# Kernel optimization log

Hardware: AMD Instinct MI355X
Metric: run time of the kernel (lower is better)

Reference implementation:

```python
import jax, jax.numpy as jnp
import numpy as np

B, L, V, E, H, K, T = 256, 49, 10000, 512, 512, 512, 15


def setup_inputs() -> dict:
    key = jax.random.key(0)
    ks = jax.random.split(key, 16)
    s = 0.02
    return {
        "features": jax.random.normal(ks[0], (B, L, K), dtype=jnp.float32),
        "captions": jax.random.randint(ks[1], (B, T), 0, V),
        "emb": jax.random.normal(ks[2], (V, E), dtype=jnp.float32) * s,
        "Wq": jax.random.normal(ks[3], (H, H), dtype=jnp.float32) * s,
        "bq": jnp.zeros((H,), jnp.float32),
        "Uk": jax.random.normal(ks[4], (H, K), dtype=jnp.float32) * s,
        "bk": jnp.zeros((H,), jnp.float32),
        "Va": jax.random.normal(ks[5], (1, H), dtype=jnp.float32) * s,
        "bva": jnp.zeros((1,), jnp.float32),
        "W0": jax.random.normal(ks[6], (H, K), dtype=jnp.float32) * s,
        "b0": jnp.zeros((H,), jnp.float32),
        "Wih": jax.random.normal(ks[7], (3 * H, E + H), dtype=jnp.float32) * s,
        "bih": jnp.zeros((3 * H,), jnp.float32),
        "Whh": jax.random.normal(ks[8], (3 * H, H), dtype=jnp.float32) * s,
        "bhh": jnp.zeros((3 * H,), jnp.float32),
        "W1": jax.random.normal(ks[9], (V, H), dtype=jnp.float32) * s,
        "b1": jnp.zeros((V,), jnp.float32),
    }


def reference(features, captions, emb, Wq, bq, Uk, bk, Va, bva, W0, b0, Wih, bih, Whh, bhh, W1, b1):
    # embeddings: [B, T, E]
    embeddings = emb[captions]
    # precompute key projection for additive attention: [B, L, H]
    keys_proj = jnp.einsum("blk,hk->blh", features, Uk) + bk

    def step(h, emb_t):  # h: [B,H], emb_t: [B,E]
        q = h @ Wq.T + bq                                  # [B, H]
        scores = jnp.tanh(q[:, None, :] + keys_proj) @ Va.T + bva  # [B, L, 1]
        w = jax.nn.softmax(scores, axis=1)                 # [B, L, 1]
        ctx = jnp.sum(w * features, axis=1)                # [B, K]
        ctx = ctx @ W0.T + b0                              # [B, H]
        x = jnp.concatenate([emb_t, ctx], axis=-1)         # [B, E+H]
        gi = x @ Wih.T + bih                               # [B, 3H]
        gh = h @ Whh.T + bhh                               # [B, 3H]
        i_r, i_z, i_n = jnp.split(gi, 3, axis=-1)
        h_r, h_z, h_n = jnp.split(gh, 3, axis=-1)
        r = jax.nn.sigmoid(i_r + h_r)
        z = jax.nn.sigmoid(i_z + h_z)
        n = jnp.tanh(i_n + r * h_n)
        h_new = (1.0 - z) * n + z * h
        out = h_new @ W1.T + b1                            # [B, V]
        return h_new, out

    h0 = jnp.zeros((features.shape[0], H), features.dtype)
    _, outs = jax.lax.scan(step, h0, jnp.swapaxes(embeddings, 0, 1))  # [T, B, V]
    return jnp.swapaxes(outs, 0, 1)  # [B, T, V]
```

## Files before the change

kernel.cpp:

```cpp
#include <hip/hip_runtime.h>
#include <hip/hip_bf16.h>
#include <math.h>

#define B_ 256
#define L_ 49
#define V_ 10000
#define E_ 512
#define H_ 512
#define K_ 512
#define T_ 15

typedef __bf16 bf16x8 __attribute__((ext_vector_type(8)));
typedef float f32x4 __attribute__((ext_vector_type(4)));

#define AS1 __attribute__((address_space(1)))
#define AS3 __attribute__((address_space(3)))

__device__ __forceinline__ float tanh_fast(float x)
{
    const float ax = fabsf(x);
    const float e = __expf(2.f * ax);
    const float t = 1.f - 2.f / (e + 1.f);
    return copysignf(t, x);
}

struct CvtSegs {
    const float* src[6];
    __hip_bfloat16* dst[6];
    int blk_end[6];
};

__global__ __launch_bounds__(256) void cvt_multi_kernel(CvtSegs s)
{
    const int blk = blockIdx.x;
    int seg = 0;
    while (blk >= s.blk_end[seg]) ++seg;
    const int base = seg ? s.blk_end[seg - 1] : 0;
    const int i = (blk - base) * 256 + threadIdx.x;
    const float4 v = ((const float4*)s.src[seg])[i];
    __hip_bfloat16 o[4];
    o[0] = (__hip_bfloat16)v.x; o[1] = (__hip_bfloat16)v.y;
    o[2] = (__hip_bfloat16)v.z; o[3] = (__hip_bfloat16)v.w;
    *(ushort4*)(s.dst[seg] + (size_t)i * 4) = *(ushort4*)o;
}

__global__ __launch_bounds__(256) void transpose_cast_kernel(
    const float* __restrict__ in, __hip_bfloat16* __restrict__ out, int R, int Cc)
{
    __shared__ float tile[32][33];
    const int tr0 = blockIdx.y * 32, tc0 = blockIdx.x * 32;
    const int tx = threadIdx.x & 31, ty = threadIdx.x >> 5;
#pragma unroll
    for (int i = 0; i < 32; i += 8)
        tile[ty + i][tx] = in[(size_t)(tr0 + ty + i) * Cc + tc0 + tx];
    __syncthreads();
#pragma unroll
    for (int i = 0; i < 32; i += 8)
        out[(size_t)(tc0 + ty + i) * R + tr0 + tx] = (__hip_bfloat16)tile[tx][ty + i];
}

__global__ __launch_bounds__(256) void bfull_kernel(
    const float* __restrict__ Wih, const float* __restrict__ b0,
    const float* __restrict__ bih, float* __restrict__ bfull)
{
    const int i = blockIdx.x * 256 + threadIdx.x;
    if (i >= 3 * H_) return;
    const float* wrow = Wih + (size_t)i * (E_ + H_) + E_;
    float acc = bih[i];
    for (int j = 0; j < H_; ++j) acc += wrow[j] * b0[j];
    bfull[i] = acc;
}

__global__ __launch_bounds__(128) void emb_gather_kernel(
    const int* __restrict__ caps, const float* __restrict__ emb,
    __hip_bfloat16* __restrict__ out)
{
    const int r = blockIdx.x;
    const int t = r >> 8;
    const int b = r & 255;
    const int cap = caps[(size_t)b * T_ + t];
    const int e = threadIdx.x * 4;
    const float4 v = *(const float4*)(emb + (size_t)cap * E_ + e);
    __hip_bfloat16 o[4];
    o[0] = (__hip_bfloat16)v.x; o[1] = (__hip_bfloat16)v.y;
    o[2] = (__hip_bfloat16)v.z; o[3] = (__hip_bfloat16)v.w;
    *(ushort4*)(out + (size_t)r * E_ + e) = *(ushort4*)o;
}

template <typename OutT>
__global__ __launch_bounds__(256) void gemm_bf16_nt128_kernel(
    const __hip_bfloat16* __restrict__ A, const __hip_bfloat16* __restrict__ Bw,
    const float* __restrict__ bias, OutT* __restrict__ C,
    int N, int Kd, int lda, int ldb, int ldc, int nby)
{
    int wg = blockIdx.x;
    {
        const int nwg = gridDim.x;
        const int q = nwg >> 3, r = nwg & 7;
        const int xcd = wg & 7, idx = wg >> 3;
        wg = (xcd < r ? xcd * (q + 1) : r * (q + 1) + (xcd - r) * q) + idx;
    }
    const int by = wg % nby;
    const int bx = wg / nby;
    const int row0 = by * 128;
    const int col0 = bx * 128;

    __shared__ __hip_bfloat16 Asl[128 * 64];
    __shared__ __hip_bfloat16 Bsl[128 * 64];
    const int tid  = threadIdx.x;
    const int lane = tid & 63;
    const int w    = tid >> 6;
    const int wm   = w >> 1, wn = w & 1;

    const int srow = tid >> 3;
    const int scol = (tid & 7) << 3;

    const int lr = lane & 15;
    const int lk = (lane >> 4) << 3;

    f32x4 acc[4][4] = {};

    const __hip_bfloat16* gA = A + (size_t)(row0 + srow) * lda + scol;
    bool bv[4];
    const __hip_bfloat16* gB[4];
#pragma unroll
    for (int i = 0; i < 4; ++i) {
        const int br = col0 + i * 32 + srow;
        bv[i] = br < N;
        gB[i] = Bw + (size_t)br * ldb + scol;
    }

    for (int k0 = 0; k0 < Kd; k0 += 64) {
        __syncthreads();
#pragma unroll
        for (int i = 0; i < 4; ++i)
            __builtin_amdgcn_global_load_lds((const AS1 void*)(gA + (size_t)i * 32 * lda + k0),
                (AS3 void*)(Asl + i * 2048 + tid * 8), 16, 0, 0);
#pragma unroll
        for (int i = 0; i < 4; ++i)
            if (bv[i]) __builtin_amdgcn_global_load_lds((const AS1 void*)(gB[i] + k0),
                (AS3 void*)(Bsl + i * 2048 + tid * 8), 16, 0, 0);
        __syncthreads();

#pragma unroll
        for (int ks = 0; ks < 2; ++ks) {
            bf16x8 af[4], bfr[4];
#pragma unroll
            for (int i = 0; i < 4; ++i)
                af[i] = *(const bf16x8*)(Asl + (wm * 64 + i * 16 + lr) * 64 + ks * 32 + lk);
#pragma unroll
            for (int j = 0; j < 4; ++j)
                bfr[j] = *(const bf16x8*)(Bsl + (wn * 64 + j * 16 + lr) * 64 + ks * 32 + lk);
#pragma unroll
            for (int i = 0; i < 4; ++i)
#pragma unroll
                for (int j = 0; j < 4; ++j)
                    acc[i][j] = __builtin_amdgcn_mfma_f32_16x16x32_bf16(
                        af[i], bfr[j], acc[i][j], 0, 0, 0);
        }
    }

    const int orow = (lane >> 4) << 2;
#pragma unroll
    for (int i = 0; i < 4; ++i) {
#pragma unroll
        for (int j = 0; j < 4; ++j) {
            const int col = col0 + wn * 64 + j * 16 + lr;
            if (col >= N) continue;
            const float bvv = bias ? bias[col] : 0.f;
            const int rowb = row0 + wm * 64 + i * 16 + orow;
#pragma unroll
            for (int r = 0; r < 4; ++r)
                C[(size_t)(rowb + r) * ldc + col] = (OutT)(acc[i][j][r] + bvv);
        }
    }
}

template <typename OutT, typename CinT>
__device__ __forceinline__ void gemm_nt_body(
    const __hip_bfloat16* __restrict__ A, const __hip_bfloat16* __restrict__ Bw,
    const float* __restrict__ bias, const CinT* __restrict__ Cin, int ldcin,
    OutT* __restrict__ C, int M, int N, int Kd, int lda, int ldb, int ldc,
    int bx, int by)
{
    __shared__ __hip_bfloat16 Asl[2][64 * 64];
    __shared__ __hip_bfloat16 Bsl[2][64 * 64];
    const int tid  = threadIdx.x;
    const int lane = tid & 63;
    const int w    = tid >> 6;
    const int wm   = w >> 1, wn = w & 1;
    const int row0 = by * 64;
    const int col0 = bx * 64;

    const int srow = tid >> 3;
    const int scol = (tid & 7) << 3;

    const int lr = lane & 15;
    const int lk = (lane >> 4) << 3;

    f32x4 acc[2][2] = {};

    const __hip_bfloat16* gA0 = A + (size_t)(row0 + srow) * lda + scol;
    const __hip_bfloat16* gA1 = gA0 + (size_t)32 * lda;
    const int br0 = col0 + srow, br1 = br0 + 32;
    const __hip_bfloat16* gB0 = Bw + (size_t)br0 * ldb + scol;
    const __hip_bfloat16* gB1 = gB0 + (size_t)32 * ldb;
    const bool v0 = br0 < N, v1 = br1 < N;

    auto stage = [&](int buf, int k0) {
        __builtin_amdgcn_global_load_lds((const AS1 void*)(gA0 + k0),
            (AS3 void*)(&Asl[buf][tid * 8]), 16, 0, 0);
        __builtin_amdgcn_global_load_lds((const AS1 void*)(gA1 + k0),
            (AS3 void*)(&Asl[buf][2048 + tid * 8]), 16, 0, 0);
        if (v0) __builtin_amdgcn_global_load_lds((const AS1 void*)(gB0 + k0),
            (AS3 void*)(&Bsl[buf][tid * 8]), 16, 0, 0);
        if (v1) __builtin_amdgcn_global_load_lds((const AS1 void*)(gB1 + k0),
            (AS3 void*)(&Bsl[buf][2048 + tid * 8]), 16, 0, 0);
    };

    stage(0, 0);
    __syncthreads();
    int cur = 0;
    for (int k0 = 0; k0 < Kd; k0 += 64) {
        if (k0 + 64 < Kd) stage(cur ^ 1, k0 + 64);

#pragma unroll
        for (int ks = 0; ks < 2; ++ks) {
            bf16x8 af[2], bfr[2];
#pragma unroll
            for (int i = 0; i < 2; ++i)
                af[i] = *(const bf16x8*)(&Asl[cur][(wm * 32 + i * 16 + lr) * 64 + ks * 32 + lk]);
#pragma unroll
            for (int j = 0; j < 2; ++j)
                bfr[j] = *(const bf16x8*)(&Bsl[cur][(wn * 32 + j * 16 + lr) * 64 + ks * 32 + lk]);
#pragma unroll
            for (int i = 0; i < 2; ++i)
#pragma unroll
                for (int j = 0; j < 2; ++j)
                    acc[i][j] = __builtin_amdgcn_mfma_f32_16x16x32_bf16(
                        af[i], bfr[j], acc[i][j], 0, 0, 0);
        }
        __syncthreads();
        cur ^= 1;
    }

    const int orow = (lane >> 4) << 2;
#pragma unroll
    for (int i = 0; i < 2; ++i) {
#pragma unroll
        for (int j = 0; j < 2; ++j) {
            const int col = col0 + wn * 32 + j * 16 + lr;
            if (col >= N) continue;
            const float bvv = bias ? bias[col] : 0.f;
            const int rowb = row0 + wm * 32 + i * 16 + orow;
#pragma unroll
            for (int r = 0; r < 4; ++r) {
                float v = acc[i][j][r] + bvv;
                if (Cin) v += (float)Cin[(size_t)(rowb + r) * ldcin + col];
                C[(size_t)(rowb + r) * ldc + col] = (OutT)v;
            }
        }
    }
}

__global__ __launch_bounds__(256) void gemm_gigh_kernel(
    const __hip_bfloat16* __restrict__ ctx, const __hip_bfloat16* __restrict__ Wf,
    const __hip_bfloat16* __restrict__ gi_emb_t,
    const __hip_bfloat16* __restrict__ hb, const __hip_bfloat16* __restrict__ Whh,
    const float* __restrict__ bhh,
    __hip_bfloat16* __restrict__ gi, __hip_bfloat16* __restrict__ gh)
{
    if (blockIdx.z == 0)
        gemm_nt_body<__hip_bfloat16, __hip_bfloat16>(
            ctx, Wf, nullptr, gi_emb_t, 3 * H_, gi,
            B_, 3 * H_, K_, K_, K_, 3 * H_, blockIdx.x, blockIdx.y);
    else
        gemm_nt_body<__hip_bfloat16, float>(
            hb, Whh, bhh, (const float*)nullptr, 0, gh,
            B_, 3 * H_, H_, H_, H_, 3 * H_, blockIdx.x, blockIdx.y);
}

__global__ __launch_bounds__(512) void attn_gru_kernel(
    const __hip_bfloat16* __restrict__ gi, const __hip_bfloat16* __restrict__ gh,
    float* __restrict__ h, __hip_bfloat16* __restrict__ hb,
    __hip_bfloat16* __restrict__ h_all, int tprev,
    const __hip_bfloat16* __restrict__ WqT, const float* __restrict__ bq,
    const __hip_bfloat16* __restrict__ kp, const __hip_bfloat16* __restrict__ feat,
    const float* __restrict__ Va, const float* __restrict__ bva,
    __hip_bfloat16* __restrict__ ctx)
{
    const int b = blockIdx.x;
    const int tid = threadIdx.x;
    const int lane = tid & 63;
    const int wave = tid >> 6;
    __shared__ float hb_s[H_];
    __shared__ float q_part[8][H_];
    __shared__ float q_s[H_];
    __shared__ float s_sc[64];
    __shared__ float s_w[64];

    if (tprev >= 0) {
        const int j = tid;
        const size_t o = (size_t)b * (3 * H_) + j;
        const float ir = (float)gi[o],           hr = (float)gh[o];
        const float iz = (float)gi[o + H_],      hz = (float)gh[o + H_];
        const float in_ = (float)gi[o + 2 * H_], hn = (float)gh[o + 2 * H_];
        const float rr = 1.f / (1.f + expf(-(ir + hr)));
        const float zz = 1.f / (1.f + expf(-(iz + hz)));
        const float nn = tanhf(in_ + rr * hn);
        const size_t hi = (size_t)b * H_ + j;
        const float hnew = (1.f - zz) * nn + zz * h[hi];
        h[hi] = hnew;
        hb_s[j] = hnew;
        const __hip_bfloat16 hv = (__hip_bfloat16)hnew;
        hb[hi] = hv;
        h_all[((size_t)b * T_ + tprev) * H_ + j] = hv;
    } else {
        hb_s[tid] = 0.f;
    }
    __syncthreads();

    {
        const int j0 = lane * 8;
        float accq[8] = {};
        const __hip_bfloat16* wbase = WqT + (size_t)(wave * 64) * H_ + j0;
#pragma unroll 16
        for (int k = 0; k < 64; ++k) {
            const float hv = hb_s[wave * 64 + k];
            const bf16x8 wv = *(const bf16x8*)(wbase + (size_t)k * H_);
#pragma unroll
            for (int i = 0; i < 8; ++i) accq[i] = fmaf(hv, (float)wv[i], accq[i]);
        }
#pragma unroll
        for (int i = 0; i < 8; ++i) q_part[wave][j0 + i] = accq[i];
    }
    __syncthreads();
    {
        const int j = tid;
        float s = bq[j];
#pragma unroll
        for (int w2 = 0; w2 < 8; ++w2) s += q_part[w2][j];
        q_s[j] = s;
    }
    __syncthreads();

    float qr[8], va[8];
#pragma unroll
    for (int i = 0; i < 8; ++i) {
        qr[i] = q_s[lane * 8 + i];
        va[i] = Va[lane * 8 + i];
    }

    for (int l = wave; l < L_; l += 8) {
        const bf16x8 kv = *(const bf16x8*)(kp + ((size_t)b * L_ + l) * H_ + lane * 8);
        float s = 0.f;
#pragma unroll
        for (int i = 0; i < 8; ++i) s += tanh_fast(qr[i] + (float)kv[i]) * va[i];
#pragma unroll
        for (int off = 32; off > 0; off >>= 1) s += __shfl_xor(s, off, 64);
        if (lane == 0) s_sc[l] = s + bva[0];
    }
    __syncthreads();

    if (wave == 0) {
        const float v = (lane < L_) ? s_sc[lane] : -1e30f;
        float m = v;
#pragma unroll
        for (int off = 32; off > 0; off >>= 1) m = fmaxf(m, __shfl_xor(m, off, 64));
        const float e = (lane < L_) ? expf(v - m) : 0.f;
        float ssum = e;
#pragma unroll
        for (int off = 32; off > 0; off >>= 1) ssum += __shfl_xor(ssum, off, 64);
        if (lane < L_) s_w[lane] = e / ssum;
    }
    __syncthreads();

    {
        float acc0 = 0.f;
        const __hip_bfloat16* fb = feat + (size_t)b * L_ * K_ + tid;
#pragma unroll 7
        for (int l = 0; l < L_; ++l)
            acc0 = fmaf(s_w[l], (float)fb[(size_t)l * K_], acc0);
        ctx[(size_t)b * K_ + tid] = (__hip_bfloat16)acc0;
    }
}

__global__ __launch_bounds__(256) void gru_kernel(
    const __hip_bfloat16* __restrict__ gi, const __hip_bfloat16* __restrict__ gh,
    float* __restrict__ h, __hip_bfloat16* __restrict__ hb,
    __hip_bfloat16* __restrict__ h_all, int t)
{
    const int idx = blockIdx.x * 256 + threadIdx.x;
    const int b = idx >> 9;
    const int j = idx & (H_ - 1);
    const size_t o = (size_t)b * 3 * H_ + j;
    const float ir = (float)gi[o],           hr = (float)gh[o];
    const float iz = (float)gi[o + H_],      hz = (float)gh[o + H_];
    const float in_ = (float)gi[o + 2 * H_], hn = (float)gh[o + 2 * H_];
    const float r = 1.f / (1.f + expf(-(ir + hr)));
    const float z = 1.f / (1.f + expf(-(iz + hz)));
    const float n = tanhf(in_ + r * hn);
    const float hnew = (1.f - z) * n + z * h[idx];
    h[idx] = hnew;
    const __hip_bfloat16 hv = (__hip_bfloat16)hnew;
    hb[idx] = hv;
    h_all[((size_t)b * T_ + t) * H_ + j] = hv;
}

extern "C" void kernel_launch(void* const* d_in, const int* in_sizes, int n_in,
                              void* d_out, int out_size, void* d_ws, size_t ws_size,
                              hipStream_t stream)
{
    const float* features = (const float*)d_in[0];
    const int*   captions = (const int*)d_in[1];
    const float* emb  = (const float*)d_in[2];
    const float* Wq   = (const float*)d_in[3];
    const float* bq   = (const float*)d_in[4];
    const float* Uk   = (const float*)d_in[5];
    const float* bk   = (const float*)d_in[6];
    const float* Va   = (const float*)d_in[7];
    const float* bva  = (const float*)d_in[8];
    const float* W0   = (const float*)d_in[9];
    const float* b0   = (const float*)d_in[10];
    const float* Wih  = (const float*)d_in[11];
    const float* bih  = (const float*)d_in[12];
    const float* Whh  = (const float*)d_in[13];
    const float* bhh  = (const float*)d_in[14];
    const float* W1   = (const float*)d_in[15];
    const float* b1   = (const float*)d_in[16];
    float* out = (float*)d_out;

    float* ws = (float*)d_ws;
    float* h      = ws; ws += B_ * H_;
    float* bfull  = ws; ws += 3 * H_;
    __hip_bfloat16* bws = (__hip_bfloat16*)ws;
    __hip_bfloat16* gi      = bws; bws += (size_t)B_ * 3 * H_;
    __hip_bfloat16* gh      = bws; bws += (size_t)B_ * 3 * H_;
    __hip_bfloat16* gi_emb  = bws; bws += (size_t)T_ * B_ * 3 * H_;
    __hip_bfloat16* feat_bf = bws; bws += (size_t)B_ * L_ * K_;
    __hip_bfloat16* kp_bf   = bws; bws += (size_t)B_ * L_ * H_;
    __hip_bfloat16* W1_bf   = bws; bws += (size_t)V_ * H_;
    __hip_bfloat16* Uk_bf   = bws; bws += (size_t)H_ * K_;
    __hip_bfloat16* WqT_bf  = bws; bws += (size_t)H_ * H_;
    __hip_bfloat16* W0T_bf  = bws; bws += (size_t)K_ * H_;
    __hip_bfloat16* Wih_bf  = bws; bws += (size_t)3 * H_ * (E_ + H_);
    __hip_bfloat16* Whh_bf  = bws; bws += (size_t)3 * H_ * H_;
    __hip_bfloat16* Wfused  = bws; bws += (size_t)3 * H_ * K_;
    __hip_bfloat16* emb_all = bws; bws += (size_t)T_ * B_ * E_;
    __hip_bfloat16* hb      = bws; bws += (size_t)B_ * H_;
    __hip_bfloat16* ctx_bf  = bws; bws += (size_t)B_ * K_;
    __hip_bfloat16* h_all   = bws; bws += (size_t)B_ * T_ * H_;

    hipMemsetAsync(h, 0, (size_t)B_ * H_ * sizeof(float), stream);
    hipMemsetAsync(hb, 0, (size_t)B_ * H_ * sizeof(__hip_bfloat16), stream);

    const dim3 blk(256);

    {
        CvtSegs s;
        s.src[0] = features; s.dst[0] = feat_bf;
        s.src[1] = W1;       s.dst[1] = W1_bf;
        s.src[2] = Uk;       s.dst[2] = Uk_bf;
        s.src[3] = Wih;      s.dst[3] = Wih_bf;
        s.src[4] = Whh;      s.dst[4] = Whh_bf;
        const int nb[5] = {
            B_ * L_ * K_ / 1024, V_ * H_ / 1024, H_ * K_ / 1024,
            3 * H_ * (E_ + H_) / 1024, 3 * H_ * H_ / 1024 };
        int cum = 0;
        for (int i = 0; i < 5; ++i) { cum += nb[i]; s.blk_end[i] = cum; }
        s.src[5] = nullptr; s.dst[5] = nullptr; s.blk_end[5] = cum + 1;
        cvt_multi_kernel<<<dim3(cum), blk, 0, stream>>>(s);
    }
    transpose_cast_kernel<<<dim3(H_ / 32, H_ / 32), blk, 0, stream>>>(Wq, WqT_bf, H_, H_);
    transpose_cast_kernel<<<dim3(K_ / 32, H_ / 32), blk, 0, stream>>>(W0, W0T_bf, H_, K_);
    bfull_kernel<<<dim3((3 * H_ + 255) / 256), blk, 0, stream>>>(Wih, b0, bih, bfull);
    emb_gather_kernel<<<dim3(T_ * B_), dim3(128), 0, stream>>>(captions, emb, emb_all);

    gemm_bf16_nt128_kernel<__hip_bfloat16><<<dim3((B_ * L_ / 128) * (H_ / 128)), blk, 0, stream>>>(
        feat_bf, Uk_bf, bk, kp_bf, H_, K_, K_, K_, H_, B_ * L_ / 128);

    gemm_bf16_nt128_kernel<__hip_bfloat16><<<dim3((3 * H_ / 128) * (K_ / 128)), blk, 0, stream>>>(
        Wih_bf + E_, W0T_bf, nullptr, Wfused, K_, H_, E_ + H_, H_, K_, 3 * H_ / 128);

    gemm_bf16_nt128_kernel<__hip_bfloat16><<<dim3((T_ * B_ / 128) * (3 * H_ / 128)), blk, 0, stream>>>(
        emb_all, Wih_bf, bfull, gi_emb, 3 * H_, E_, E_, E_ + H_, 3 * H_, T_ * B_ / 128);

    for (int t = 0; t < T_; ++t) {
        attn_gru_kernel<<<dim3(B_), dim3(512), 0, stream>>>(
            gi, gh, h, hb, h_all, t - 1,
            WqT_bf, bq, kp_bf, feat_bf, Va, bva, ctx_bf);
        gemm_gigh_kernel<<<dim3(3 * H_ / 64, B_ / 64, 2), blk, 0, stream>>>(
            ctx_bf, Wfused, gi_emb + (size_t)t * B_ * 3 * H_,
            hb, Whh_bf, bhh, gi, gh);
    }
    gru_kernel<<<dim3(B_ * H_ / 256), blk, 0, stream>>>(gi, gh, h, hb, h_all, T_ - 1);

    gemm_bf16_nt128_kernel<float><<<dim3((B_ * T_ / 128) * ((V_ + 127) / 128)), blk, 0, stream>>>(
        h_all, W1_bf, b1, out, V_, H_, H_, H_, V_, B_ * T_ / 128);
}
```

Before: 770.4 us.

## Split attention step to overlap Whh GEMM with attention in one launch

The per-step work is split into three kernels: GRU update plus query projection, attention fused with the h·Whh GEMM in a single heterogeneous launch, and the context-dependent gi GEMM. Because gh depends only on h, it can run concurrently with attention blocks instead of waiting for ctx. The cost is an extra kernel launch per timestep and a round-trip of q through global memory, and attention now uses 256-thread blocks.

```diff
diff --git a/kernel.cpp b/kernel.cpp
--- a/kernel.cpp
+++ b/kernel.cpp
@@ -263,31 +263,12 @@
     }
 }
 
-__global__ __launch_bounds__(256) void gemm_gigh_kernel(
-    const __hip_bfloat16* __restrict__ ctx, const __hip_bfloat16* __restrict__ Wf,
-    const __hip_bfloat16* __restrict__ gi_emb_t,
-    const __hip_bfloat16* __restrict__ hb, const __hip_bfloat16* __restrict__ Whh,
-    const float* __restrict__ bhh,
-    __hip_bfloat16* __restrict__ gi, __hip_bfloat16* __restrict__ gh)
-{
-    if (blockIdx.z == 0)
-        gemm_nt_body<__hip_bfloat16, __hip_bfloat16>(
-            ctx, Wf, nullptr, gi_emb_t, 3 * H_, gi,
-            B_, 3 * H_, K_, K_, K_, 3 * H_, blockIdx.x, blockIdx.y);
-    else
-        gemm_nt_body<__hip_bfloat16, float>(
-            hb, Whh, bhh, (const float*)nullptr, 0, gh,
-            B_, 3 * H_, H_, H_, H_, 3 * H_, blockIdx.x, blockIdx.y);
-}
-
-__global__ __launch_bounds__(512) void attn_gru_kernel(
+__global__ __launch_bounds__(512) void gru_q_kernel(
     const __hip_bfloat16* __restrict__ gi, const __hip_bfloat16* __restrict__ gh,
     float* __restrict__ h, __hip_bfloat16* __restrict__ hb,
     __hip_bfloat16* __restrict__ h_all, int tprev,
     const __hip_bfloat16* __restrict__ WqT, const float* __restrict__ bq,
-    const __hip_bfloat16* __restrict__ kp, const __hip_bfloat16* __restrict__ feat,
-    const float* __restrict__ Va, const float* __restrict__ bva,
-    __hip_bfloat16* __restrict__ ctx)
+    float* __restrict__ q)
 {
     const int b = blockIdx.x;
     const int tid = threadIdx.x;
@@ -295,9 +276,6 @@
     const int wave = tid >> 6;
     __shared__ float hb_s[H_];
     __shared__ float q_part[8][H_];
-    __shared__ float q_s[H_];
-    __shared__ float s_sc[64];
-    __shared__ float s_w[64];
 
     if (tprev >= 0) {
         const int j = tid;
@@ -340,18 +318,43 @@
         float s = bq[j];
 #pragma unroll
         for (int w2 = 0; w2 < 8; ++w2) s += q_part[w2][j];
-        q_s[j] = s;
-    }
-    __syncthreads();
+        q[(size_t)b * H_ + j] = s;
+    }
+}
+
+__global__ __launch_bounds__(256) void attn_gh_kernel(
+    const float* __restrict__ q, const __hip_bfloat16* __restrict__ kp,
+    const __hip_bfloat16* __restrict__ feat, const float* __restrict__ Va,
+    const float* __restrict__ bva, __hip_bfloat16* __restrict__ ctx,
+    const __hip_bfloat16* __restrict__ hb, const __hip_bfloat16* __restrict__ Whh,
+    const float* __restrict__ bhh, __hip_bfloat16* __restrict__ gh)
+{
+    const int bid = blockIdx.x;
+    if (bid >= B_) {
+        const int task = bid - B_;
+        const int bx = task % 24;
+        const int by = task / 24;
+        gemm_nt_body<__hip_bfloat16, float>(
+            hb, Whh, bhh, (const float*)nullptr, 0, gh,
+            B_, 3 * H_, H_, H_, H_, 3 * H_, bx, by);
+        return;
+    }
+
+    const int b = bid;
+    const int tid = threadIdx.x;
+    const int lane = tid & 63;
+    const int wave = tid >> 6;
+    __shared__ float s_sc[64];
+    __shared__ float s_w[64];
 
     float qr[8], va[8];
 #pragma unroll
     for (int i = 0; i < 8; ++i) {
-        qr[i] = q_s[lane * 8 + i];
+        qr[i] = q[(size_t)b * H_ + lane * 8 + i];
         va[i] = Va[lane * 8 + i];
     }
 
-    for (int l = wave; l < L_; l += 8) {
+    for (int l = wave; l < L_; l += 4) {
         const bf16x8 kv = *(const bf16x8*)(kp + ((size_t)b * L_ + l) * H_ + lane * 8);
         float s = 0.f;
 #pragma unroll
@@ -376,13 +379,26 @@
     __syncthreads();
 
     {
-        float acc0 = 0.f;
-        const __hip_bfloat16* fb = feat + (size_t)b * L_ * K_ + tid;
+        float acc0 = 0.f, acc1 = 0.f;
+        const __hip_bfloat16* fb = feat + (size_t)b * L_ * K_;
 #pragma unroll 7
-        for (int l = 0; l < L_; ++l)
-            acc0 = fmaf(s_w[l], (float)fb[(size_t)l * K_], acc0);
-        ctx[(size_t)b * K_ + tid] = (__hip_bfloat16)acc0;
-    }
+        for (int l = 0; l < L_; ++l) {
+            const float wl = s_w[l];
+            acc0 = fmaf(wl, (float)fb[(size_t)l * K_ + tid], acc0);
+            acc1 = fmaf(wl, (float)fb[(size_t)l * K_ + tid + 256], acc1);
+        }
+        ctx[(size_t)b * K_ + tid]       = (__hip_bfloat16)acc0;
+        ctx[(size_t)b * K_ + tid + 256] = (__hip_bfloat16)acc1;
+    }
+}
+
+__global__ __launch_bounds__(256) void gi_kernel(
+    const __hip_bfloat16* __restrict__ ctx, const __hip_bfloat16* __restrict__ Wf,
+    const __hip_bfloat16* __restrict__ gi_emb_t, __hip_bfloat16* __restrict__ gi)
+{
+    gemm_nt_body<__hip_bfloat16, __hip_bfloat16>(
+        ctx, Wf, nullptr, gi_emb_t, 3 * H_, gi,
+        B_, 3 * H_, K_, K_, K_, 3 * H_, blockIdx.x, blockIdx.y);
 }
 
 __global__ __launch_bounds__(256) void gru_kernel(
@@ -433,6 +449,7 @@
     float* ws = (float*)d_ws;
     float* h      = ws; ws += B_ * H_;
     float* bfull  = ws; ws += 3 * H_;
+    float* qbuf   = ws; ws += B_ * H_;
     __hip_bfloat16* bws = (__hip_bfloat16*)ws;
     __hip_bfloat16* gi      = bws; bws += (size_t)B_ * 3 * H_;
     __hip_bfloat16* gh      = bws; bws += (size_t)B_ * 3 * H_;
@@ -486,12 +503,13 @@
         emb_all, Wih_bf, bfull, gi_emb, 3 * H_, E_, E_, E_ + H_, 3 * H_, T_ * B_ / 128);
 
     for (int t = 0; t < T_; ++t) {
-        attn_gru_kernel<<<dim3(B_), dim3(512), 0, stream>>>(
-            gi, gh, h, hb, h_all, t - 1,
-            WqT_bf, bq, kp_bf, feat_bf, Va, bva, ctx_bf);
-        gemm_gigh_kernel<<<dim3(3 * H_ / 64, B_ / 64, 2), blk, 0, stream>>>(
-            ctx_bf, Wfused, gi_emb + (size_t)t * B_ * 3 * H_,
-            hb, Whh_bf, bhh, gi, gh);
+        gru_q_kernel<<<dim3(B_), dim3(512), 0, stream>>>(
+            gi, gh, h, hb, h_all, t - 1, WqT_bf, bq, qbuf);
+        attn_gh_kernel<<<dim3(B_ + 96), blk, 0, stream>>>(
+            qbuf, kp_bf, feat_bf, Va, bva, ctx_bf,
+            hb, Whh_bf, bhh, gh);
+        gi_kernel<<<dim3(24, 4), blk, 0, stream>>>(
+            ctx_bf, Wfused, gi_emb + (size_t)t * B_ * 3 * H_, gi);
     }
     gru_kernel<<<dim3(B_ * H_ / 256), blk, 0, stream>>>(gi, gh, h, hb, h_all, T_ - 1);
 
```

New measurement: 870.9 us. +13.0%, slower.
